# Kernel optimization log

Hardware: AMD Instinct MI355X
Metric: run time of the kernel (lower is better)

## Reference

```python
import jax, jax.numpy as jnp
import numpy as np

THRESHOLD = 6.0  # bnb MatmulLtState outlier threshold


def setup_inputs() -> dict:
    key = jax.random.key(0)
    k1, k2, k3, k4, k5 = jax.random.split(key, 5)
    B, S, DIN, DOUT = 4, 2048, 4096, 16384
    x = jax.random.normal(k1, (B, S, DIN), dtype=jnp.float32).astype(jnp.float16)
    # inject a few outlier feature columns (|x| > threshold) so the LLM.int8()
    # mixed-precision decomposition path is actually exercised
    out_cols = jax.random.randint(k5, (8,), 0, DIN)
    x = x.at[:, :, out_cols].multiply(10.0)
    # CB: int8 codebook values stored as fp16 (bnb keeps them as int8; math is identical)
    CB = jnp.round(jax.random.uniform(k2, (DOUT, DIN), minval=-127.0, maxval=127.0)).astype(jnp.float16)
    SCB = jax.random.uniform(k3, (DOUT, 1), minval=0.5, maxval=2.0).astype(jnp.float16)
    bias = (jax.random.normal(k4, (DOUT,)) * 0.01).astype(jnp.float16)
    return {"x": x, "CB": CB, "SCB": SCB, "bias": bias}


def _llm_int8_matmul(x, CB, SCB, bias, threshold):
    # forward: weight = CB * SCB / 127 (dequantized fp16 weight), then bnb's
    # mixed int8 matmul with outlier-column decomposition (has_fp16_weights=True)
    W = CB.astype(jnp.float32) * SCB.astype(jnp.float32) / 127.0  # [DOUT, DIN]
    xf = x.astype(jnp.float32)
    lead = xf.shape[:-1]
    X = xf.reshape(-1, xf.shape[-1])  # [N, DIN]

    # outlier columns: any row has |x| > threshold in that feature column
    col_out = (jnp.abs(X) > threshold).any(axis=0)  # [DIN] bool
    X_out = jnp.where(col_out[None, :], X, 0.0)      # fp16-path activations
    X_in = jnp.where(col_out[None, :], 0.0, X)       # int8-path activations

    # per-row (per-token) absmax int8 quantization of inlier activations
    sx = jnp.maximum(jnp.max(jnp.abs(X_in), axis=1, keepdims=True), 1e-8)  # [N,1]
    Xq = jnp.clip(jnp.round(X_in * (127.0 / sx)), -127.0, 127.0)

    # per-output-row absmax int8 quantization of the (dequantized) weight
    sw = jnp.maximum(jnp.max(jnp.abs(W), axis=1, keepdims=True), 1e-8)  # [DOUT,1]
    Wq = jnp.clip(jnp.round(W * (127.0 / sw)), -127.0, 127.0)

    # int8 GEMM (emulated in fp32) + dequant with outer product of scales
    out = (Xq @ Wq.T) * (sx * sw.T) * (1.0 / (127.0 * 127.0))  # [N, DOUT]
    # fp16 outlier path: only the outlier weight columns participate
    out = out + X_out @ jnp.where(col_out[None, :], W, 0.0).T
    out = out + bias.astype(jnp.float32)[None, :]
    return out.reshape(*lead, W.shape[0]).astype(jnp.float16)


def reference(x, CB, SCB, bias):
    return _llm_int8_matmul(x, CB, SCB, bias, THRESHOLD)
```

## Files before the change

### kernel.cpp

```cpp
#include <hip/hip_runtime.h>
#include <hip/hip_fp16.h>
#include <stdint.h>

typedef int v4i __attribute__((ext_vector_type(4)));

__device__ __forceinline__ void gld_lds16(const void* g, void* l) {
    __builtin_amdgcn_global_load_lds(
        (const __attribute__((address_space(1))) void*)g,
        (__attribute__((address_space(3))) void*)l,
        16, 0, 0);
}

#define ENDBAR() do { __builtin_amdgcn_s_barrier(); __builtin_amdgcn_sched_barrier(0); } while (0)
#define VMC(n)   asm volatile("s_waitcnt vmcnt(" #n ")" ::: "memory")
#define VMLG0()  asm volatile("s_waitcnt vmcnt(0) lgkmcnt(0)" ::: "memory")

__global__ __launch_bounds__(256) void k_flags(const float* __restrict__ x,
                                               unsigned int* __restrict__ flags,
                                               int total4, int DIN) {
    int idx = blockIdx.x * blockDim.x + threadIdx.x;
    int stride = gridDim.x * blockDim.x;
    int dmask = DIN - 1;
    for (int i = idx; i < total4; i += stride) {
        float4 v = ((const float4*)x)[i];
        int base = i * 4;
        if (fabsf(v.x) > 6.0f) atomicOr(&flags[(base + 0) & dmask], 1u);
        if (fabsf(v.y) > 6.0f) atomicOr(&flags[(base + 1) & dmask], 1u);
        if (fabsf(v.z) > 6.0f) atomicOr(&flags[(base + 2) & dmask], 1u);
        if (fabsf(v.w) > 6.0f) atomicOr(&flags[(base + 3) & dmask], 1u);
    }
}

__global__ __launch_bounds__(256) void k_build(const unsigned int* __restrict__ flags,
                                               unsigned char* __restrict__ bmask,
                                               int* __restrict__ ncols,
                                               int* __restrict__ cols, int DIN) {
    __shared__ int wcnt[4];
    __shared__ int base;
    int tid = threadIdx.x, lane = tid & 63, wid = tid >> 6;
    if (tid == 0) base = 0;
    __syncthreads();
    for (int c0 = 0; c0 < DIN; c0 += 256) {
        int c = c0 + tid;
        bool p = (c < DIN) && (flags[c] != 0u);
        if (c < DIN) bmask[c] = p ? 1 : 0;
        unsigned long long m = __ballot(p);
        int wpre = __popcll(m & ((1ull << lane) - 1ull));
        if (lane == 0) wcnt[wid] = __popcll(m);
        __syncthreads();
        int pre = 0;
        for (int w = 0; w < wid; w++) pre += wcnt[w];
        if (p) cols[base + pre + wpre] = c;
        __syncthreads();
        if (tid == 0) base += wcnt[0] + wcnt[1] + wcnt[2] + wcnt[3];
        __syncthreads();
    }
    if (tid == 0) *ncols = base;
}

__global__ __launch_bounds__(256) void k_quantx(const float* __restrict__ x,
                                                const unsigned char* __restrict__ bmask,
                                                signed char* __restrict__ Xq,
                                                float* __restrict__ sx, int DIN) {
    int row = blockIdx.x;
    int tid = threadIdx.x, lane = tid & 63, wid = tid >> 6;
    const float* xr = x + (size_t)row * DIN;
    float f[16];
    #pragma unroll
    for (int j = 0; j < 4; j++) {
        float4 v = ((const float4*)xr)[tid * 4 + j];
        f[4*j] = v.x; f[4*j+1] = v.y; f[4*j+2] = v.z; f[4*j+3] = v.w;
    }
    uint4 bm4 = ((const uint4*)bmask)[tid];
    const unsigned char* bm = (const unsigned char*)&bm4;
    float m = 0.0f;
    #pragma unroll
    for (int j = 0; j < 16; j++) {
        if (bm[j]) f[j] = 0.0f;
        m = fmaxf(m, fabsf(f[j]));
    }
    #pragma unroll
    for (int off = 32; off >= 1; off >>= 1) m = fmaxf(m, __shfl_xor(m, off));
    __shared__ float red[4];
    if (lane == 0) red[wid] = m;
    __syncthreads();
    m = fmaxf(fmaxf(red[0], red[1]), fmaxf(red[2], red[3]));
    float sxv = fmaxf(m, 1e-8f);
    if (Xq) {
        float scale = 127.0f / sxv;
        int qi[16];
        #pragma unroll
        for (int j = 0; j < 16; j++) {
            float r = rintf(f[j] * scale);
            r = fminf(127.0f, fmaxf(-127.0f, r));
            qi[j] = (int)r;
        }
        int4 ov;
        ov.x = (qi[0]&0xff) | ((qi[1]&0xff)<<8) | ((qi[2]&0xff)<<16) | ((qi[3]&0xff)<<24);
        ov.y = (qi[4]&0xff) | ((qi[5]&0xff)<<8) | ((qi[6]&0xff)<<16) | ((qi[7]&0xff)<<24);
        ov.z = (qi[8]&0xff) | ((qi[9]&0xff)<<8) | ((qi[10]&0xff)<<16) | ((qi[11]&0xff)<<24);
        ov.w = (qi[12]&0xff) | ((qi[13]&0xff)<<8) | ((qi[14]&0xff)<<16) | ((qi[15]&0xff)<<24);
        ((int4*)(Xq + (size_t)row * DIN))[tid] = ov;
    }
    if (tid == 0) sx[row] = sxv;
}

__global__ __launch_bounds__(256) void k_quantw(const float* __restrict__ CB,
                                                const float* __restrict__ SCB,
                                                signed char* __restrict__ Wq,
                                                float* __restrict__ sw, int DIN) {
    int row = blockIdx.x;
    int tid = threadIdx.x, lane = tid & 63, wid = tid >> 6;
    float scb = SCB[row];
    const float* cr = CB + (size_t)row * DIN;
    float w[16];
    #pragma unroll
    for (int j = 0; j < 4; j++) {
        float4 v = ((const float4*)cr)[tid * 4 + j];
        w[4*j]   = v.x * scb / 127.0f;
        w[4*j+1] = v.y * scb / 127.0f;
        w[4*j+2] = v.z * scb / 127.0f;
        w[4*j+3] = v.w * scb / 127.0f;
    }
    float m = 0.0f;
    #pragma unroll
    for (int j = 0; j < 16; j++) m = fmaxf(m, fabsf(w[j]));
    #pragma unroll
    for (int off = 32; off >= 1; off >>= 1) m = fmaxf(m, __shfl_xor(m, off));
    __shared__ float red[4];
    if (lane == 0) red[wid] = m;
    __syncthreads();
    m = fmaxf(fmaxf(red[0], red[1]), fmaxf(red[2], red[3]));
    float swv = fmaxf(m, 1e-8f);
    if (Wq) {
        float scale = 127.0f / swv;
        int qi[16];
        #pragma unroll
        for (int j = 0; j < 16; j++) {
            float r = rintf(w[j] * scale);
            r = fminf(127.0f, fmaxf(-127.0f, r));
            qi[j] = (int)r;
        }
        int4 ov;
        ov.x = (qi[0]&0xff) | ((qi[1]&0xff)<<8) | ((qi[2]&0xff)<<16) | ((qi[3]&0xff)<<24);
        ov.y = (qi[4]&0xff) | ((qi[5]&0xff)<<8) | ((qi[6]&0xff)<<16) | ((qi[7]&0xff)<<24);
        ov.z = (qi[8]&0xff) | ((qi[9]&0xff)<<8) | ((qi[10]&0xff)<<16) | ((qi[11]&0xff)<<24);
        ov.w = (qi[12]&0xff) | ((qi[13]&0xff)<<8) | ((qi[14]&0xff)<<16) | ((qi[15]&0xff)<<24);
        ((int4*)(Wq + (size_t)row * DIN))[tid] = ov;
    }
    if (tid == 0) sw[row] = swv;
}

__global__ __launch_bounds__(256) void k_outpanels(
    const float* __restrict__ x, const float* __restrict__ CB,
    const float* __restrict__ SCB, const int* __restrict__ ncols,
    const int* __restrict__ cols, float* __restrict__ Xout, float* __restrict__ Wout,
    int Nrows, int DOUT, int DIN)
{
    int nc = *ncols;
    int ncl = nc < 16 ? nc : 16;
    int idx = blockIdx.x * 256 + threadIdx.x;
    int row = idx >> 4, c = idx & 15;
    if (row >= Nrows + DOUT) return;
    float v = 0.0f;
    if (row < Nrows) {
        if (c < ncl) v = x[(size_t)row * DIN + cols[c]];
        Xout[row * 16 + c] = v;
    } else {
        int j = row - Nrows;
        if (c < ncl) v = CB[(size_t)j * DIN + cols[c]] * SCB[j] / 127.0f;
        Wout[j * 16 + c] = v;
    }
}

__global__ __launch_bounds__(512) void k_gemm8(
    const signed char* __restrict__ Xq, const signed char* __restrict__ Wq,
    const float* __restrict__ sx, const float* __restrict__ sw,
    const float* __restrict__ x, const float* __restrict__ CB,
    const float* __restrict__ SCB, const float* __restrict__ bias,
    const float* __restrict__ Xout, const float* __restrict__ Wout,
    const int* __restrict__ ncols, const int* __restrict__ cols,
    float* __restrict__ out, int Nrows, int DOUT, int DIN)
{
    __shared__ __align__(16) char LDS[131072];

    const int tid = threadIdx.x, lane = tid & 63, wid = tid >> 6;
    const int wm = wid >> 2, wn = wid & 3;

    int nwg = gridDim.x, bid = blockIdx.x;
    int swzb;
    if ((nwg & 7) == 0) { int cpx = nwg >> 3; swzb = (bid & 7) * cpx + (bid >> 3); }
    else swzb = bid;
    int mtiles = Nrows >> 8;
    int mt = swzb % mtiles, ntl = swzb / mtiles;
    int brow = mt << 8, bcol = ntl << 8;

    const int o0 = 16 * ((lane >> 4) ^ ((lane >> 1) & 7));
    const int o1 = o0 ^ 64;
    const int aRow = (wm * 128 + (lane & 15)) * 128;
    const int bRow = (wn * 64 + (lane & 15)) * 128;

    const int stRow = wid * 8 + (lane >> 3);
    const int stCol = 16 * ((lane & 7) ^ (((wid & 1) << 2) + (lane >> 4)));
    const signed char* aSrc = Xq + (size_t)(brow + stRow) * DIN + stCol;
    const signed char* bSrc = Wq + (size_t)(bcol + stRow) * DIN + stCol;
    const int ldsW = wid * 1024;

    v4i acc[8][4] = {};
    v4i a0[8], a1[8], b0[4], b1[4];

    const int nt = DIN >> 7;
    const int NIT = nt >> 1;

#define STAGE_HALF(srcBase, matOff, bf, h, kc)                                   \
    do { _Pragma("unroll")                                                        \
      for (int q = 0; q < 2; q++) {                                               \
        int seg = 2*(h) + q;                                                      \
        gld_lds16((srcBase) + (size_t)seg * 64 * DIN + (kc),                      \
                  &LDS[(matOff) + (bf)*32768 + seg*8192 + ldsW]);                 \
      }                                                                           \
    } while (0)

#define DS_A(dst, bf, miB)                                                        \
    do { _Pragma("unroll")                                                        \
      for (int mi = 0; mi < 4; mi++) {                                            \
        int ro = (bf)*32768 + aRow + ((miB) + mi) * 2048;                         \
        dst[mi*2+0] = *(const v4i*)&LDS[ro + o0];                                 \
        dst[mi*2+1] = *(const v4i*)&LDS[ro + o1];                                 \
      }                                                                           \
    } while (0)

#define DS_B(dst, bf, niB)                                                        \
    do { _Pragma("unroll")                                                        \
      for (int ni = 0; ni < 2; ni++) {                                            \
        int ro = 65536 + (bf)*32768 + bRow + ((niB) + ni) * 2048;                 \
        dst[ni*2+0] = *(const v4i*)&LDS[ro + o0];                                 \
        dst[ni*2+1] = *(const v4i*)&LDS[ro + o1];                                 \
      }                                                                           \
    } while (0)

#define QUAD(A8, B4, accM, accN)                                                  \
    do { __builtin_amdgcn_s_setprio(1); _Pragma("unroll")                         \
      for (int mi = 0; mi < 4; mi++) { _Pragma("unroll")                          \
        for (int ni = 0; ni < 2; ni++) { _Pragma("unroll")                        \
          for (int ks = 0; ks < 2; ks++)                                          \
            acc[(accM)+mi][(accN)+ni] = __builtin_amdgcn_mfma_i32_16x16x64_i8(    \
                A8[mi*2+ks], B4[ni*2+ks], acc[(accM)+mi][(accN)+ni], 0, 0, 0);    \
        } }                                                                       \
      __builtin_amdgcn_s_setprio(0);                                              \
    } while (0)

    STAGE_HALF(aSrc, 0,     0, 0, 0);
    STAGE_HALF(aSrc, 0,     0, 1, 0);
    STAGE_HALF(bSrc, 65536, 0, 0, 0);
    STAGE_HALF(bSrc, 65536, 0, 1, 0);
    STAGE_HALF(aSrc, 0,     1, 0, 128);
    STAGE_HALF(aSrc, 0,     1, 1, 128);
    VMC(4);
    ENDBAR();

    for (int it = 0; it < NIT; ++it) {
        int t = 2 * it;
        int kB1 = (t + 1) << 7;
        int tA2 = t + 2; if (tA2 > nt - 1) tA2 = nt - 1;
        int kA2 = tA2 << 7;
        int tA3 = t + 3; if (tA3 > nt - 1) tA3 = nt - 1;
        int kA3 = tA3 << 7;

        STAGE_HALF(bSrc, 65536, 1, 0, kB1);
        DS_B(b0, 0, 0); DS_A(a0, 0, 0);
        QUAD(a0, b0, 0, 0);
        ENDBAR();
        STAGE_HALF(bSrc, 65536, 1, 1, kB1);
        DS_A(a1, 0, 4);
        QUAD(a1, b0, 4, 0);
        ENDBAR();
        STAGE_HALF(aSrc, 0, 0, 0, kA2);
        DS_B(b1, 0, 2);
        QUAD(a1, b1, 4, 2);
        ENDBAR();
        STAGE_HALF(aSrc, 0, 0, 1, kA2);
        QUAD(a0, b1, 0, 2);
        VMC(4);
        ENDBAR();
        STAGE_HALF(bSrc, 65536, 0, 0, kA2);
        DS_B(b0, 1, 0); DS_A(a0, 1, 0);
        QUAD(a0, b0, 0, 0);
        ENDBAR();
        STAGE_HALF(bSrc, 65536, 0, 1, kA2);
        DS_A(a1, 1, 4);
        QUAD(a1, b0, 4, 0);
        ENDBAR();
        STAGE_HALF(aSrc, 0, 1, 0, kA3);
        DS_B(b1, 1, 2);
        QUAD(a1, b1, 4, 2);
        ENDBAR();
        STAGE_HALF(aSrc, 0, 1, 1, kA3);
        QUAD(a0, b1, 0, 2);
        VMC(4);
        ENDBAR();
    }
    VMLG0();
    ENDBAR();

    int nc = *ncols;
    int ncl = nc < 16 ? nc : 16;
    float* Xo = (float*)&LDS[0];
    float* Wo = (float*)&LDS[65536];
    for (int idx = tid; idx < 4096; idx += 512) {
        int i = idx >> 4, c = idx & 15;
        Xo[i * 17 + c] = Xout[(size_t)(brow + i) * 16 + c];
        Wo[i * 17 + c] = Wout[(size_t)(bcol + i) * 16 + c];
    }
    __syncthreads();

    float sww[4], bzz[4];
    #pragma unroll
    for (int ni = 0; ni < 4; ni++) {
        int gcol = bcol + wn * 64 + ni * 16 + (lane & 15);
        sww[ni] = sw[gcol];
        bzz[ni] = bias[gcol];
    }

    #pragma unroll
    for (int h = 0; h < 2; h++) {
        float vout[4][4][4];
        #pragma unroll
        for (int mi = 0; mi < 4; mi++) {
            int row = wm * 128 + (h * 4 + mi) * 16 + (lane >> 4) * 4;
            #pragma unroll
            for (int r = 0; r < 4; r++) {
                float sxv = sx[brow + row + r];
                #pragma unroll
                for (int ni = 0; ni < 4; ni++)
                    vout[mi][ni][r] =
                        ((float)acc[h * 4 + mi][ni][r] * (sxv * sww[ni])) * (1.0f / 16129.0f);
            }
        }
        for (int c = 0; c < ncl; c++) {
            float wo[4];
            #pragma unroll
            for (int ni = 0; ni < 4; ni++)
                wo[ni] = Wo[(wn * 64 + ni * 16 + (lane & 15)) * 17 + c];
            #pragma unroll
            for (int mi = 0; mi < 4; mi++) {
                int row = wm * 128 + (h * 4 + mi) * 16 + (lane >> 4) * 4;
                #pragma unroll
                for (int r = 0; r < 4; r++) {
                    float xo = Xo[(row + r) * 17 + c];
                    #pragma unroll
                    for (int ni = 0; ni < 4; ni++)
                        vout[mi][ni][r] += xo * wo[ni];
                }
            }
        }
        #pragma unroll
        for (int mi = 0; mi < 4; mi++) {
            #pragma unroll
            for (int ni = 0; ni < 4; ni++) {
                int gcol = bcol + wn * 64 + ni * 16 + (lane & 15);
                #pragma unroll
                for (int r = 0; r < 4; r++) {
                    int grow = brow + wm * 128 + (h * 4 + mi) * 16 + (lane >> 4) * 4 + r;
                    float v = vout[mi][ni][r];
                    for (int c = 16; c < nc; c++) {
                        int col = cols[c];
                        v += x[(size_t)grow * DIN + col] *
                             (CB[(size_t)gcol * DIN + col] * SCB[gcol] / 127.0f);
                    }
                    v += bzz[ni];
                    v = __half2float(__float2half(v));
                    out[(size_t)grow * DOUT + gcol] = v;
                }
            }
        }
    }
#undef STAGE_HALF
#undef DS_A
#undef DS_B
#undef QUAD
}

template<int FLY>
__global__ __launch_bounds__(256) void k_gemm(
    const signed char* __restrict__ Xq, const signed char* __restrict__ Wq,
    const float* __restrict__ sx, const float* __restrict__ sw,
    const float* __restrict__ x, const float* __restrict__ CB,
    const float* __restrict__ SCB, const float* __restrict__ bias,
    const unsigned char* __restrict__ bmask,
    const int* __restrict__ ncols, const int* __restrict__ cols,
    float* __restrict__ out, int Nrows, int DOUT, int DIN)
{
    __shared__ __align__(16) signed char Asm[128 * 64];
    __shared__ __align__(16) signed char Bsm[128 * 64];

    int nwg = gridDim.x;
    int bid = blockIdx.x;
    int swzb;
    if ((nwg & 7) == 0) { int cpx = nwg >> 3; swzb = (bid & 7) * cpx + (bid >> 3); }
    else swzb = bid;
    int mtiles = Nrows >> 7;
    int mt = swzb % mtiles;
    int nt = swzb / mtiles;
    int brow = mt << 7, bcol = nt << 7;

    int tid = threadIdx.x, lane = tid & 63, wid = tid >> 6;
    int wr = wid >> 1, wc = wid & 1;

    v4i acc[4][4] = {};

    int arow = wr * 64 + (lane & 15);
    int brl  = wc * 64 + (lane & 15);
    int kc   = (lane >> 4) * 16;

    if constexpr (FLY == 0) {
        int srow = lane >> 2;
        int scol = (lane & 3) * 16;
        const signed char* ga0 = Xq + (size_t)(brow + wid * 16 + srow) * DIN + scol;
        const signed char* ga1 = Xq + (size_t)(brow + (wid + 4) * 16 + srow) * DIN + scol;
        const signed char* gb0 = Wq + (size_t)(bcol + wid * 16 + srow) * DIN + scol;
        const signed char* gb1 = Wq + (size_t)(bcol + (wid + 4) * 16 + srow) * DIN + scol;
        signed char* la0 = &Asm[wid * 1024];
        signed char* la1 = &Asm[(wid + 4) * 1024];
        signed char* lb0 = &Bsm[wid * 1024];
        signed char* lb1 = &Bsm[(wid + 4) * 1024];

        for (int k0 = 0; k0 < DIN; k0 += 64) {
            gld_lds16(ga0 + k0, la0);
            gld_lds16(ga1 + k0, la1);
            gld_lds16(gb0 + k0, lb0);
            gld_lds16(gb1 + k0, lb1);
            __syncthreads();
            v4i a[4], b[4];
            #pragma unroll
            for (int mi = 0; mi < 4; mi++) a[mi] = *(const v4i*)&Asm[(arow + mi * 16) * 64 + kc];
            #pragma unroll
            for (int ni = 0; ni < 4; ni++) b[ni] = *(const v4i*)&Bsm[(brl + ni * 16) * 64 + kc];
            #pragma unroll
            for (int mi = 0; mi < 4; mi++)
                #pragma unroll
                for (int ni = 0; ni < 4; ni++)
                    acc[mi][ni] = __builtin_amdgcn_mfma_i32_16x16x64_i8(a[mi], b[ni], acc[mi][ni], 0, 0, 0);
            __syncthreads();
        }
    } else {
        int ra = tid >> 1, ca = (tid & 1) * 32;
        const float* xrow = x  + (size_t)(brow + ra) * DIN + ca;
        const float* crow = CB + (size_t)(bcol + ra) * DIN + ca;
        float xscale = 127.0f / sx[brow + ra];
        float scb    = SCB[bcol + ra];
        float wscale = 127.0f / sw[bcol + ra];
        signed char* lda = &Asm[ra * 64 + ca];
        signed char* ldb = &Bsm[ra * 64 + ca];

        for (int k0 = 0; k0 < DIN; k0 += 64) {
            float xa[32], wb[32];
            #pragma unroll
            for (int j = 0; j < 8; j++) {
                float4 v = ((const float4*)(xrow + k0))[j];
                xa[4*j] = v.x; xa[4*j+1] = v.y; xa[4*j+2] = v.z; xa[4*j+3] = v.w;
                float4 u = ((const float4*)(crow + k0))[j];
                wb[4*j] = u.x; wb[4*j+1] = u.y; wb[4*j+2] = u.z; wb[4*j+3] = u.w;
            }
            uint4 bm0 = *(const uint4*)(bmask + k0 + ca);
            uint4 bm1 = *(const uint4*)(bmask + k0 + ca + 16);
            const unsigned char* bmp0 = (const unsigned char*)&bm0;
            const unsigned char* bmp1 = (const unsigned char*)&bm1;
            int qa[32], qb[32];
            #pragma unroll
            for (int j = 0; j < 32; j++) {
                float fx = xa[j];
                if ((j < 16 ? bmp0[j] : bmp1[j - 16])) fx = 0.0f;
                float rx = rintf(fx * xscale);
                qa[j] = (int)fminf(127.0f, fmaxf(-127.0f, rx));
                float wv = wb[j] * scb / 127.0f;
                float rw = rintf(wv * wscale);
                qb[j] = (int)fminf(127.0f, fmaxf(-127.0f, rw));
            }
            int4 pa0, pa1, pb0, pb1;
            #pragma unroll
            for (int g = 0; g < 8; g++) {
                int vpk = (qa[4*g]&0xff) | ((qa[4*g+1]&0xff)<<8) | ((qa[4*g+2]&0xff)<<16) | ((qa[4*g+3]&0xff)<<24);
                if (g < 4) ((int*)&pa0)[g] = vpk; else ((int*)&pa1)[g-4] = vpk;
                int wpk = (qb[4*g]&0xff) | ((qb[4*g+1]&0xff)<<8) | ((qb[4*g+2]&0xff)<<16) | ((qb[4*g+3]&0xff)<<24);
                if (g < 4) ((int*)&pb0)[g] = wpk; else ((int*)&pb1)[g-4] = wpk;
            }
            __syncthreads();
            *(int4*)lda = pa0; *(int4*)(lda + 16) = pa1;
            *(int4*)ldb = pb0; *(int4*)(ldb + 16) = pb1;
            __syncthreads();
            v4i a[4], b[4];
            #pragma unroll
            for (int mi = 0; mi < 4; mi++) a[mi] = *(const v4i*)&Asm[(arow + mi * 16) * 64 + kc];
            #pragma unroll
            for (int ni = 0; ni < 4; ni++) b[ni] = *(const v4i*)&Bsm[(brl + ni * 16) * 64 + kc];
            #pragma unroll
            for (int mi = 0; mi < 4; mi++)
                #pragma unroll
                for (int ni = 0; ni < 4; ni++)
                    acc[mi][ni] = __builtin_amdgcn_mfma_i32_16x16x64_i8(a[mi], b[ni], acc[mi][ni], 0, 0, 0);
        }
        __syncthreads();
    }

    int nc = *ncols;
    int ncl = nc < 16 ? nc : 16;
    float* Xo = (float*)Asm;
    float* Wo = (float*)Bsm;
    for (int idx = tid; idx < 2048; idx += 256) {
        int i = idx >> 4, c = idx & 15;
        if (c < ncl) {
            int col = cols[c];
            Xo[idx] = x[(size_t)(brow + i) * DIN + col];
            Wo[idx] = CB[(size_t)(bcol + i) * DIN + col] * SCB[bcol + i] / 127.0f;
        }
    }
    __syncthreads();

    #pragma unroll
    for (int mi = 0; mi < 4; mi++) {
        #pragma unroll
        for (int ni = 0; ni < 4; ni++) {
            int rl0 = wr * 64 + mi * 16 + (lane >> 4) * 4;
            int cl  = wc * 64 + ni * 16 + (lane & 15);
            int gcol = bcol + cl;
            float swv = sw[gcol];
            float bz = bias[gcol];
            #pragma unroll
            for (int r = 0; r < 4; r++) {
                int grow = brow + rl0 + r;
                float v = ((float)acc[mi][ni][r] * (sx[grow] * swv)) * (1.0f / 16129.0f);
                float osum = 0.0f;
                for (int c = 0; c < ncl; c++)
                    osum += Xo[(rl0 + r) * 16 + c] * Wo[cl * 16 + c];
                for (int c = 16; c < nc; c++) {
                    int col = cols[c];
                    osum += x[(size_t)grow * DIN + col] *
                            (CB[(size_t)gcol * DIN + col] * SCB[gcol] / 127.0f);
                }
                v = v + osum;
                v = v + bz;
                v = __half2float(__float2half(v));
                out[(size_t)grow * DOUT + gcol] = v;
            }
        }
    }
}

static constexpr size_t FLAGS_OFF = 0;
static constexpr size_t BMASK_OFF = 16384;
static constexpr size_t NCOLS_OFF = 20480;
static constexpr size_t COLS_OFF  = 20544;
static constexpr size_t SX_OFF    = 36992;
static constexpr size_t SW_OFF    = 69760;
static constexpr size_t DYN_OFF   = 262144;

extern "C" void kernel_launch(void* const* d_in, const int* in_sizes, int n_in,
                              void* d_out, int out_size, void* d_ws, size_t ws_size,
                              hipStream_t stream) {
    const float* x    = (const float*)d_in[0];
    const float* CB   = (const float*)d_in[1];
    const float* SCB  = (const float*)d_in[2];
    const float* bias = (const float*)d_in[3];

    int DOUT  = in_sizes[2];
    int DIN   = in_sizes[1] / DOUT;
    int Nrows = in_sizes[0] / DIN;

    char* ws = (char*)d_ws;
    unsigned int* flags = (unsigned int*)(ws + FLAGS_OFF);
    unsigned char* bmask = (unsigned char*)(ws + BMASK_OFF);
    int* ncols = (int*)(ws + NCOLS_OFF);
    int* cols  = (int*)(ws + COLS_OFF);
    float* sx  = (float*)(ws + SX_OFF);
    float* sw  = (float*)(ws + SW_OFF);

    size_t off = DYN_OFF;
    float* Xout = (float*)(ws + off); off += (size_t)Nrows * 16 * 4;
    float* Wout = (float*)(ws + off); off += (size_t)DOUT * 16 * 4;
    signed char* Xq = (signed char*)(ws + off); off += (size_t)Nrows * DIN;
    signed char* Wq = (signed char*)(ws + off); off += (size_t)DOUT * DIN;
    size_t need = off;
    float* out = (float*)d_out;

    bool bigws = ws_size >= need;
    bool can8  = bigws && (Nrows % 256 == 0) && (DOUT % 256 == 0) && (DIN % 256 == 0);

    hipMemsetAsync(ws + FLAGS_OFF, 0, 16384, stream);
    k_flags<<<2048, 256, 0, stream>>>(x, flags, Nrows * DIN / 4, DIN);
    k_build<<<1, 256, 0, stream>>>(flags, bmask, ncols, cols, DIN);
    k_quantx<<<Nrows, 256, 0, stream>>>(x, bmask, bigws ? Xq : nullptr, sx, DIN);
    k_quantw<<<DOUT, 256, 0, stream>>>(CB, SCB, bigws ? Wq : nullptr, sw, DIN);

    if (can8) {
        int total_threads = (Nrows + DOUT) * 16;
        int nblk = (total_threads + 255) / 256;
        k_outpanels<<<nblk, 256, 0, stream>>>(
            x, CB, SCB, ncols, cols, Xout, Wout, Nrows, DOUT, DIN);
        int ngrid = (Nrows / 256) * (DOUT / 256);
        k_gemm8<<<ngrid, 512, 0, stream>>>(Xq, Wq, sx, sw, x, CB, SCB, bias,
                                           Xout, Wout, ncols, cols, out, Nrows, DOUT, DIN);
    } else if (bigws) {
        int ngrid = (Nrows / 128) * (DOUT / 128);
        k_gemm<0><<<ngrid, 256, 0, stream>>>(Xq, Wq, sx, sw, x, CB, SCB, bias,
                                             bmask, ncols, cols, out, Nrows, DOUT, DIN);
    } else {
        int ngrid = (Nrows / 128) * (DOUT / 128);
        k_gemm<1><<<ngrid, 256, 0, stream>>>(nullptr, nullptr, sx, sw, x, CB, SCB, bias,
                                             bmask, ncols, cols, out, Nrows, DOUT, DIN);
    }
}
```

Before: 807.2 us.

## Split 256x256 int8 GEMM tile across 16 waves instead of 8

The int8 GEMM block grows from 512 to 1024 threads. Each wave now owns a 64x64 output sub-tile instead of 128x64, which halves the per-wave accumulator and fragment registers. Staging is redone so each wave loads two 16-byte chunks per matrix per k-step, and the swizzle and pipeline phases are adjusted to match. The aim is more waves per CU to hide latency, at the cost of each wave reusing its A and B fragments less and doing more LDS reads per MFMA.

```diff
diff --git a/kernel.cpp b/kernel.cpp
--- a/kernel.cpp
+++ b/kernel.cpp
@@ -173,7 +173,7 @@
     }
 }
 
-__global__ __launch_bounds__(512) void k_gemm8(
+__global__ __launch_bounds__(1024, 4) void k_gemm8(
     const signed char* __restrict__ Xq, const signed char* __restrict__ Wq,
     const float* __restrict__ sx, const float* __restrict__ sw,
     const float* __restrict__ x, const float* __restrict__ CB,
@@ -197,107 +197,95 @@
 
     const int o0 = 16 * ((lane >> 4) ^ ((lane >> 1) & 7));
     const int o1 = o0 ^ 64;
-    const int aRow = (wm * 128 + (lane & 15)) * 128;
-    const int bRow = (wn * 64 + (lane & 15)) * 128;
+    const int aRowB = (wm * 64 + (lane & 15)) * 128;
+    const int bRowB = (wn * 64 + (lane & 15)) * 128;
 
     const int stRow = wid * 8 + (lane >> 3);
-    const int stCol = 16 * ((lane & 7) ^ (((wid & 1) << 2) + (lane >> 4)));
+    const int stCol = 16 * ((lane & 7) ^ ((wid * 4 + (lane >> 4)) & 7));
     const signed char* aSrc = Xq + (size_t)(brow + stRow) * DIN + stCol;
     const signed char* bSrc = Wq + (size_t)(bcol + stRow) * DIN + stCol;
     const int ldsW = wid * 1024;
 
-    v4i acc[8][4] = {};
-    v4i a0[8], a1[8], b0[4], b1[4];
+    v4i acc[4][4] = {};
+    v4i a[8], b[4];
 
     const int nt = DIN >> 7;
     const int NIT = nt >> 1;
 
-#define STAGE_HALF(srcBase, matOff, bf, h, kc)                                   \
+#define STAGE_A(bf, kc)                                                          \
+    do {                                                                          \
+        gld_lds16(aSrc + (kc), &LDS[(bf)*32768 + ldsW]);                          \
+        gld_lds16(aSrc + (size_t)128 * DIN + (kc),                                \
+                  &LDS[(bf)*32768 + 16384 + ldsW]);                               \
+    } while (0)
+
+#define STAGE_B(bf, kc)                                                          \
+    do {                                                                          \
+        gld_lds16(bSrc + (kc), &LDS[65536 + (bf)*32768 + ldsW]);                  \
+        gld_lds16(bSrc + (size_t)128 * DIN + (kc),                                \
+                  &LDS[65536 + (bf)*32768 + 16384 + ldsW]);                       \
+    } while (0)
+
+#define DS_A(bf)                                                                  \
     do { _Pragma("unroll")                                                        \
-      for (int q = 0; q < 2; q++) {                                               \
-        int seg = 2*(h) + q;                                                      \
-        gld_lds16((srcBase) + (size_t)seg * 64 * DIN + (kc),                      \
-                  &LDS[(matOff) + (bf)*32768 + seg*8192 + ldsW]);                 \
+      for (int mi = 0; mi < 4; mi++) {                                            \
+        int ro = (bf)*32768 + aRowB + mi * 2048;                                  \
+        a[mi*2+0] = *(const v4i*)&LDS[ro + o0];                                   \
+        a[mi*2+1] = *(const v4i*)&LDS[ro + o1];                                   \
       }                                                                           \
     } while (0)
 
-#define DS_A(dst, bf, miB)                                                        \
+#define DS_B(bf, p)                                                               \
     do { _Pragma("unroll")                                                        \
-      for (int mi = 0; mi < 4; mi++) {                                            \
-        int ro = (bf)*32768 + aRow + ((miB) + mi) * 2048;                         \
-        dst[mi*2+0] = *(const v4i*)&LDS[ro + o0];                                 \
-        dst[mi*2+1] = *(const v4i*)&LDS[ro + o1];                                 \
+      for (int nj = 0; nj < 2; nj++) {                                            \
+        int ro = 65536 + (bf)*32768 + bRowB + ((p)*2 + nj) * 2048;                \
+        b[nj*2+0] = *(const v4i*)&LDS[ro + o0];                                   \
+        b[nj*2+1] = *(const v4i*)&LDS[ro + o1];                                   \
       }                                                                           \
     } while (0)
 
-#define DS_B(dst, bf, niB)                                                        \
-    do { _Pragma("unroll")                                                        \
-      for (int ni = 0; ni < 2; ni++) {                                            \
-        int ro = 65536 + (bf)*32768 + bRow + ((niB) + ni) * 2048;                 \
-        dst[ni*2+0] = *(const v4i*)&LDS[ro + o0];                                 \
-        dst[ni*2+1] = *(const v4i*)&LDS[ro + o1];                                 \
-      }                                                                           \
-    } while (0)
-
-#define QUAD(A8, B4, accM, accN)                                                  \
+#define QUADP(p)                                                                  \
     do { __builtin_amdgcn_s_setprio(1); _Pragma("unroll")                         \
       for (int mi = 0; mi < 4; mi++) { _Pragma("unroll")                          \
-        for (int ni = 0; ni < 2; ni++) { _Pragma("unroll")                        \
+        for (int nj = 0; nj < 2; nj++) { _Pragma("unroll")                        \
           for (int ks = 0; ks < 2; ks++)                                          \
-            acc[(accM)+mi][(accN)+ni] = __builtin_amdgcn_mfma_i32_16x16x64_i8(    \
-                A8[mi*2+ks], B4[ni*2+ks], acc[(accM)+mi][(accN)+ni], 0, 0, 0);    \
+            acc[mi][(p)*2+nj] = __builtin_amdgcn_mfma_i32_16x16x64_i8(            \
+                a[mi*2+ks], b[nj*2+ks], acc[mi][(p)*2+nj], 0, 0, 0);              \
         } }                                                                       \
       __builtin_amdgcn_s_setprio(0);                                              \
     } while (0)
 
-    STAGE_HALF(aSrc, 0,     0, 0, 0);
-    STAGE_HALF(aSrc, 0,     0, 1, 0);
-    STAGE_HALF(bSrc, 65536, 0, 0, 0);
-    STAGE_HALF(bSrc, 65536, 0, 1, 0);
-    STAGE_HALF(aSrc, 0,     1, 0, 128);
-    STAGE_HALF(aSrc, 0,     1, 1, 128);
-    VMC(4);
+    STAGE_A(0, 0);
+    STAGE_B(0, 0);
+    STAGE_A(1, 128);
+    VMC(2);
     ENDBAR();
 
     for (int it = 0; it < NIT; ++it) {
         int t = 2 * it;
         int kB1 = (t + 1) << 7;
-        int tA2 = t + 2; if (tA2 > nt - 1) tA2 = nt - 1;
-        int kA2 = tA2 << 7;
-        int tA3 = t + 3; if (tA3 > nt - 1) tA3 = nt - 1;
-        int kA3 = tA3 << 7;
-
-        STAGE_HALF(bSrc, 65536, 1, 0, kB1);
-        DS_B(b0, 0, 0); DS_A(a0, 0, 0);
-        QUAD(a0, b0, 0, 0);
+        int t2 = t + 2; if (t2 > nt - 1) t2 = nt - 1;
+        int kA2 = t2 << 7;
+        int t3 = t + 3; if (t3 > nt - 1) t3 = nt - 1;
+        int kA3 = t3 << 7;
+
+        STAGE_B(1, kB1);
+        DS_A(0); DS_B(0, 0);
+        QUADP(0);
         ENDBAR();
-        STAGE_HALF(bSrc, 65536, 1, 1, kB1);
-        DS_A(a1, 0, 4);
-        QUAD(a1, b0, 4, 0);
+        STAGE_A(0, kA2);
+        DS_B(0, 1);
+        QUADP(1);
+        VMC(2);
         ENDBAR();
-        STAGE_HALF(aSrc, 0, 0, 0, kA2);
-        DS_B(b1, 0, 2);
-        QUAD(a1, b1, 4, 2);
+        STAGE_B(0, kA2);
+        DS_A(1); DS_B(1, 0);
+        QUADP(0);
         ENDBAR();
-        STAGE_HALF(aSrc, 0, 0, 1, kA2);
-        QUAD(a0, b1, 0, 2);
-        VMC(4);
-        ENDBAR();
-        STAGE_HALF(bSrc, 65536, 0, 0, kA2);
-        DS_B(b0, 1, 0); DS_A(a0, 1, 0);
-        QUAD(a0, b0, 0, 0);
-        ENDBAR();
-        STAGE_HALF(bSrc, 65536, 0, 1, kA2);
-        DS_A(a1, 1, 4);
-        QUAD(a1, b0, 4, 0);
-        ENDBAR();
-        STAGE_HALF(aSrc, 0, 1, 0, kA3);
-        DS_B(b1, 1, 2);
-        QUAD(a1, b1, 4, 2);
-        ENDBAR();
-        STAGE_HALF(aSrc, 0, 1, 1, kA3);
-        QUAD(a0, b1, 0, 2);
-        VMC(4);
+        STAGE_A(1, kA3);
+        DS_B(1, 1);
+        QUADP(1);
+        VMC(2);
         ENDBAR();
     }
     VMLG0();
@@ -307,7 +295,7 @@
     int ncl = nc < 16 ? nc : 16;
     float* Xo = (float*)&LDS[0];
     float* Wo = (float*)&LDS[65536];
-    for (int idx = tid; idx < 4096; idx += 512) {
+    for (int idx = tid; idx < 4096; idx += 1024) {
         int i = idx >> 4, c = idx & 15;
         Xo[i * 17 + c] = Xout[(size_t)(brow + i) * 16 + c];
         Wo[i * 17 + c] = Wout[(size_t)(bcol + i) * 16 + c];
@@ -322,63 +310,61 @@
         bzz[ni] = bias[gcol];
     }
 
-    #pragma unroll
-    for (int h = 0; h < 2; h++) {
-        float vout[4][4][4];
+    float vout[4][4][4];
+    #pragma unroll
+    for (int mi = 0; mi < 4; mi++) {
+        int row = wm * 64 + mi * 16 + (lane >> 4) * 4;
+        #pragma unroll
+        for (int r = 0; r < 4; r++) {
+            float sxv = sx[brow + row + r];
+            #pragma unroll
+            for (int ni = 0; ni < 4; ni++)
+                vout[mi][ni][r] =
+                    ((float)acc[mi][ni][r] * (sxv * sww[ni])) * (1.0f / 16129.0f);
+        }
+    }
+    for (int c = 0; c < ncl; c++) {
+        float wo[4];
+        #pragma unroll
+        for (int ni = 0; ni < 4; ni++)
+            wo[ni] = Wo[(wn * 64 + ni * 16 + (lane & 15)) * 17 + c];
         #pragma unroll
         for (int mi = 0; mi < 4; mi++) {
-            int row = wm * 128 + (h * 4 + mi) * 16 + (lane >> 4) * 4;
+            int row = wm * 64 + mi * 16 + (lane >> 4) * 4;
             #pragma unroll
             for (int r = 0; r < 4; r++) {
-                float sxv = sx[brow + row + r];
+                float xo = Xo[(row + r) * 17 + c];
                 #pragma unroll
                 for (int ni = 0; ni < 4; ni++)
-                    vout[mi][ni][r] =
-                        ((float)acc[h * 4 + mi][ni][r] * (sxv * sww[ni])) * (1.0f / 16129.0f);
+                    vout[mi][ni][r] += xo * wo[ni];
             }
         }
-        for (int c = 0; c < ncl; c++) {
-            float wo[4];
-            #pragma unroll
-            for (int ni = 0; ni < 4; ni++)
-                wo[ni] = Wo[(wn * 64 + ni * 16 + (lane & 15)) * 17 + c];
-            #pragma unroll
-            for (int mi = 0; mi < 4; mi++) {
-                int row = wm * 128 + (h * 4 + mi) * 16 + (lane >> 4) * 4;
-                #pragma unroll
-                for (int r = 0; r < 4; r++) {
-                    float xo = Xo[(row + r) * 17 + c];
-                    #pragma unroll
-                    for (int ni = 0; ni < 4; ni++)
-                        vout[mi][ni][r] += xo * wo[ni];
+    }
+    #pragma unroll
+    for (int mi = 0; mi < 4; mi++) {
+        #pragma unroll
+        for (int ni = 0; ni < 4; ni++) {
+            int gcol = bcol + wn * 64 + ni * 16 + (lane & 15);
+            #pragma unroll
+            for (int r = 0; r < 4; r++) {
+                int grow = brow + wm * 64 + mi * 16 + (lane >> 4) * 4 + r;
+                float v = vout[mi][ni][r];
+                for (int c = 16; c < nc; c++) {
+                    int col = cols[c];
+                    v += x[(size_t)grow * DIN + col] *
+                         (CB[(size_t)gcol * DIN + col] * SCB[gcol] / 127.0f);
                 }
+                v += bzz[ni];
+                v = __half2float(__float2half(v));
+                out[(size_t)grow * DOUT + gcol] = v;
             }
         }
-        #pragma unroll
-        for (int mi = 0; mi < 4; mi++) {
-            #pragma unroll
-            for (int ni = 0; ni < 4; ni++) {
-                int gcol = bcol + wn * 64 + ni * 16 + (lane & 15);
-                #pragma unroll
-                for (int r = 0; r < 4; r++) {
-                    int grow = brow + wm * 128 + (h * 4 + mi) * 16 + (lane >> 4) * 4 + r;
-                    float v = vout[mi][ni][r];
-                    for (int c = 16; c < nc; c++) {
-                        int col = cols[c];
-                        v += x[(size_t)grow * DIN + col] *
-                             (CB[(size_t)gcol * DIN + col] * SCB[gcol] / 127.0f);
-                    }
-                    v += bzz[ni];
-                    v = __half2float(__float2half(v));
-                    out[(size_t)grow * DOUT + gcol] = v;
-                }
-            }
-        }
-    }
-#undef STAGE_HALF
+    }
+#undef STAGE_A
+#undef STAGE_B
 #undef DS_A
 #undef DS_B
-#undef QUAD
+#undef QUADP
 }
 
 template<int FLY>
@@ -598,8 +584,8 @@
         k_outpanels<<<nblk, 256, 0, stream>>>(
             x, CB, SCB, ncols, cols, Xout, Wout, Nrows, DOUT, DIN);
         int ngrid = (Nrows / 256) * (DOUT / 256);
-        k_gemm8<<<ngrid, 512, 0, stream>>>(Xq, Wq, sx, sw, x, CB, SCB, bias,
-                                           Xout, Wout, ncols, cols, out, Nrows, DOUT, DIN);
+        k_gemm8<<<ngrid, 1024, 0, stream>>>(Xq, Wq, sx, sw, x, CB, SCB, bias,
+                                            Xout, Wout, ncols, cols, out, Nrows, DOUT, DIN);
     } else if (bigws) {
         int ngrid = (Nrows / 128) * (DOUT / 128);
         k_gemm<0><<<ngrid, 256, 0, stream>>>(Xq, Wq, sx, sw, x, CB, SCB, bias,
```

Result: slower. 1.238 ms (+53.4%).
